# Performance work log

Hardware: AMD Instinct MI355X
Metric: run time of the kernel (lower is better)

The kernel has to match this reference:

```python
import jax, jax.numpy as jnp
import numpy as np

D = 4
P_PIX = 13   # 2*R+1, R=6
R_PIX = 6
P_REG = 7    # R+1
DIRATE = 2   # min(4, (20-0)//15 + 1) for ref_index=[0,18], current_ind=20, dil_int=15


def correlate(t, r, P, d):
    """SpatialCorrelationSampler(kernel_size=1, patch_size=P, dilation_patch=d).
    t, r: [b,c,h,w] -> [b,P*P,h,w] ; corr[n=(i*P+j)] uses r shifted by ((i-R)*d,(j-R)*d)."""
    b, c, h, w = t.shape
    Rr = (P - 1) // 2
    pad = Rr * d
    rp = jnp.pad(r, ((0, 0), (0, 0), (pad, pad), (pad, pad)))
    # [b,c,N,h,w] stack of shifted views (zero-padded borders)
    shifts = jnp.stack([rp[:, :, i * d:i * d + h, j * d:j * d + w]
                        for i in range(P) for j in range(P)], axis=2)
    return jnp.einsum('bcyx,bcnyx->bnyx', t, shifts)


def deform_im2col(r, offset, P):
    """Deformable im2col with one shared (x,y) offset per output pixel.
    r: [b,c,h,w], offset: [b,h,w,2] (x in [...,0], y in [...,1]) -> [b,c,P*P,h,w].
    Bilinear sampling with zero outside the image."""
    b, c, h, w = r.shape
    Rr = (P - 1) // 2
    N = P * P
    ky, kx = jnp.meshgrid(jnp.arange(-Rr, Rr + 1), jnp.arange(-Rr, Rr + 1), indexing='ij')
    ky = ky.reshape(-1).astype(r.dtype)
    kx = kx.reshape(-1).astype(r.dtype)
    ys = jnp.arange(h, dtype=r.dtype)
    xs = jnp.arange(w, dtype=r.dtype)
    sy = offset[..., 1][:, None] + ys[None, None, :, None] + ky[None, :, None, None]  # [b,N,h,w]
    sx = offset[..., 0][:, None] + xs[None, None, None, :] + kx[None, :, None, None]
    y0 = jnp.floor(sy)
    x0 = jnp.floor(sx)
    wy = sy - y0
    wx = sx - x0
    rf = r.reshape(b, c, h * w)

    def gather(yi, xi):
        valid = ((yi >= 0) & (yi < h) & (xi >= 0) & (xi < w)).astype(r.dtype)
        idx = (jnp.clip(yi, 0, h - 1).astype(jnp.int32) * w
               + jnp.clip(xi, 0, w - 1).astype(jnp.int32)).reshape(b, 1, -1)
        vals = jnp.take_along_axis(rf, jnp.broadcast_to(idx, (b, c, N * h * w)), axis=2)
        return vals.reshape(b, c, N, h, w), valid

    v00, m00 = gather(y0, x0)
    v01, m01 = gather(y0, x0 + 1)
    v10, m10 = gather(y0 + 1, x0)
    v11, m11 = gather(y0 + 1, x0 + 1)
    w00 = ((1 - wy) * (1 - wx) * m00)[:, None]
    w01 = ((1 - wy) * wx * m01)[:, None]
    w10 = (wy * (1 - wx) * m10)[:, None]
    w11 = (wy * wx * m11)[:, None]
    return v00 * w00 + v01 * w01 + v10 * w10 + v11 * w11


def unfold(x, P):
    """F.unfold(x, kernel_size=P, padding=(P-1)//2) -> [b,c,P*P,h,w]."""
    b, c, h, w = x.shape
    Rr = (P - 1) // 2
    xp = jnp.pad(x, ((0, 0), (0, 0), (Rr, Rr), (Rr, Rr)))
    return jnp.stack([xp[:, :, i:i + h, j:j + w]
                      for i in range(P) for j in range(P)], axis=2)


def setup_inputs() -> dict:
    key = jax.random.key(0)
    ks = jax.random.split(key, 8)
    inp = {
        'feats_r0': jax.random.normal(ks[0], (2, 128, 32, 32), jnp.float32),
        'feats_r1': jax.random.normal(ks[1], (2, 128, 32, 32), jnp.float32),
        'feats_t': jax.random.normal(ks[2], (2, 128, 32, 32), jnp.float32),
        'quantized_r0': jax.random.uniform(ks[3], (2, 3, 128, 128), jnp.float32),
        'quantized_r1': jax.random.uniform(ks[4], (2, 3, 128, 128), jnp.float32),
        'feats_r_semantic0': jax.random.normal(ks[5], (2, 512, 16, 16), jnp.float32),
        'feats_r_semantic1': jax.random.normal(ks[6], (2, 512, 16, 16), jnp.float32),
        'feats_t_semantic': jax.random.normal(ks[7], (2, 512, 16, 16), jnp.float32),
        'current_ind': 20,
    }
    return inp


def reference(feats_r0, feats_r1, feats_t, quantized_r0, quantized_r1,
              feats_r_semantic0, feats_r_semantic1, feats_t_semantic, current_ind):
    b, c, h, w = feats_t.shape
    b_, c_, h_, w_ = feats_t_semantic.shape
    P, Rr, N = P_PIX, R_PIX, P_PIX * P_PIX

    # --- searching ref 0 (far in time): dilated coarse correlation -> soft offset ---
    coarse = correlate(feats_t, feats_r0, P, DIRATE)                     # [b,N,h,w]
    cs = jax.nn.softmax(coarse.reshape(b, N, h * w), axis=1).reshape(b, P, P, h, w)
    gv = jnp.arange(-Rr, Rr + 1, dtype=feats_t.dtype)
    off_x = jnp.einsum('bijyx,j->byx', cs, gv) * DIRATE
    off_y = jnp.einsum('bijyx,i->byx', cs, gv) * DIRATE
    offset = jnp.stack([off_x, off_y], axis=-1)                          # [b,h,w,2]

    col0 = deform_im2col(feats_r0, offset, P)                            # [b,c,N,h,w]
    corr0 = jnp.einsum('bcyx,bcnyx->bnyx', feats_t, col0).reshape(b, N, h * w)

    # --- recent ref 1: plain pixel + region correlation ---
    corr1 = correlate(feats_t, feats_r1, P, 1).reshape(b, N, h * w)
    region = correlate(feats_t_semantic, feats_r_semantic1, P_REG, 1).reshape(b_, P_REG * P_REG, h_ * w_)
    corr = jax.nn.softmax(region, axis=1)[:, None]                       # [b,1,49,h_*w_]

    corr_pixel = jax.nn.softmax(jnp.concatenate([corr0, corr1], axis=1), axis=1)[:, None]  # [b,1,2N,hw]

    # --- propagate colors ---
    qr0 = quantized_r0[:, :, ::D, ::D]
    qr1 = quantized_r1[:, :, ::D, ::D]
    uf0 = deform_im2col(qr0, offset, P).reshape(b, 3, N, h * w)
    uf1 = unfold(qr1, P).reshape(b, 3, N, h * w)
    image_uf = jnp.concatenate([uf0, uf1], axis=2)                       # [b,3,2N,hw]
    out = (corr_pixel * image_uf).sum(2).reshape(b, 3, h, w)
    return (out, corr)
```

## Files before the change

kernel.cpp:

```cpp
#include <hip/hip_runtime.h>
#include <math.h>

#define HH 32
#define WW 32
#define CC 128
#define PPIX 13
#define RPIX 6
#define NPIX 169
#define G14 14
#define NG 196
#define NTOT 338
#define DIRATE_ 2
#define HS 16
#define WSz 16
#define CS 512
#define PREG 7
#define RREG 3
#define NREG 49
#define QH 128
#define MAIN_BLOCKS 2048
#define REG_BLOCKS 512

__device__ __forceinline__ float wave_sum(float v) {
    #pragma unroll
    for (int s = 1; s < 64; s <<= 1) v += __shfl_xor(v, s, 64);
    return v;
}
__device__ __forceinline__ float wave_max(float v) {
    #pragma unroll
    for (int s = 1; s < 64; s <<= 1) v = fmaxf(v, __shfl_xor(v, s, 64));
    return v;
}

__global__ __launch_bounds__(256) void prep(
    const float* __restrict__ fr0, const float* __restrict__ fr1,
    const float* __restrict__ ft,  const float* __restrict__ qr0,
    const float* __restrict__ qr1, const float* __restrict__ rs1,
    const float* __restrict__ ts,
    float* __restrict__ Tr0, float* __restrict__ Tr1, float* __restrict__ Tt,
    float* __restrict__ Trs1, float* __restrict__ Tts,
    float* __restrict__ qs0, float* __restrict__ qs1)
{
    __shared__ float tile[32][33];
    const int tid = threadIdx.x;
    const int tx = tid & 31, ty = tid >> 5;
    int bid = blockIdx.x;
    if (bid < 768) {
        const int t = bid >> 8, rem = bid & 255;
        const int p0 = (rem & 31) * 32;
        const int c0 = ((rem >> 5) & 3) * 32;
        const int b  = rem >> 7;
        const float* s = (t==0 ? fr0 : t==1 ? fr1 : ft) + (size_t)b*CC*1024;
        float* d       = (t==0 ? Tr0 : t==1 ? Tr1 : Tt) + (size_t)b*CC*1024;
        #pragma unroll
        for (int i = ty; i < 32; i += 8) tile[i][tx] = s[(size_t)(c0+i)*1024 + p0+tx];
        __syncthreads();
        #pragma unroll
        for (int i = ty; i < 32; i += 8) d[(size_t)(p0+i)*CC + c0+tx] = tile[tx][i];
    } else if (bid < 1280) {
        bid -= 768;
        const int t = bid >> 8, rem = bid & 255;
        const int p0 = (rem & 7) * 32;
        const int c0 = ((rem >> 3) & 15) * 32;
        const int b  = rem >> 7;
        const float* s = (t==0 ? rs1 : ts) + (size_t)b*CS*256;
        float* d       = (t==0 ? Trs1 : Tts) + (size_t)b*CS*256;
        #pragma unroll
        for (int i = ty; i < 32; i += 8) tile[i][tx] = s[(size_t)(c0+i)*256 + p0+tx];
        __syncthreads();
        #pragma unroll
        for (int i = ty; i < 32; i += 8) d[(size_t)(p0+i)*CS + c0+tx] = tile[tx][i];
    } else {
        const int base = (bid - 1280) * 256 + tid;
        for (int e = base; e < 2*6144; e += 2048) {
            const int t = e / 6144, r2 = e % 6144;
            const int bc = r2 >> 10, yx = r2 & 1023;
            const int yy = yx >> 5, xx = yx & 31;
            const float v = (t==0 ? qr0 : qr1)[((size_t)bc*QH + yy*4)*QH + xx*4];
            (t==0 ? qs0 : qs1)[r2] = v;
        }
    }
}

__global__ __launch_bounds__(512) void colorizer_fused(
    const float* __restrict__ Tr0,
    const float* __restrict__ Tr1,
    const float* __restrict__ Tt,
    const float* __restrict__ qs0,
    const float* __restrict__ qs1,
    const float* __restrict__ Trs1,
    const float* __restrict__ Tts,
    float* __restrict__ out,
    float* __restrict__ corr_out)
{
    __shared__ __align__(16) float tvec[CS];
    __shared__ float rbuf[72];
    __shared__ float smC0[NPIX];
    __shared__ float smG[NG];
    __shared__ float smC1[NPIX];
    __shared__ float smV[NTOT];
    __shared__ float smQ0[3*NG];
    __shared__ float smQ1[3*NPIX];

    const int tid  = threadIdx.x;
    const int lane = tid & 63;
    const int wid  = tid >> 6;

    if (blockIdx.x >= REG_BLOCKS) {
        const int orig = blockIdx.x - REG_BLOCKS;
        const int bid = (orig & 7) * (MAIN_BLOCKS/8) + (orig >> 3);
        const int b   = bid >> 10;
        const int pix = bid & 1023;
        const int y = pix >> 5, x = pix & 31;

        if (tid < 32)
            ((float4*)tvec)[tid] = ((const float4*)Tt)[(size_t)b*32768 + pix*32 + tid];
        __syncthreads();

        const float4* tp  = (const float4*)tvec;
        const float4* Tr0q = (const float4*)Tr0 + (size_t)b*32768;
        const float4* Tr1q = (const float4*)Tr1 + (size_t)b*32768;
        const int q4 = lane & 3, g4 = lane >> 2;

        float4 tf[8];
        #pragma unroll
        for (int r = 0; r < 8; ++r) tf[r] = tp[q4 + r*4];

        #pragma unroll 1
        for (int set = 0; set < 2; ++set) {
            const int di = set*128 + wid*16 + g4;
            int inb = 0, yx = 0;
            if (di < NPIX) {
                const int ys = y + (di/PPIX - RPIX)*DIRATE_;
                const int xs = x + (di%PPIX - RPIX)*DIRATE_;
                inb = (ys>=0 && ys<HH && xs>=0 && xs<WW);
                yx = inb ? ys*WW+xs : 0;
            }
            const float4* rp = Tr0q + yx*32 + q4;
            float4 a; a.x=a.y=a.z=a.w=0.f;
            #pragma unroll
            for (int r = 0; r < 8; ++r) {
                const float4 rv = rp[r*4];
                a.x = fmaf(rv.x,tf[r].x,a.x); a.y = fmaf(rv.y,tf[r].y,a.y);
                a.z = fmaf(rv.z,tf[r].z,a.z); a.w = fmaf(rv.w,tf[r].w,a.w);
            }
            float s = (a.x+a.y)+(a.z+a.w);
            s += __shfl_xor(s, 1, 64); s += __shfl_xor(s, 2, 64);
            if (q4 == 0 && di < NPIX) smC0[di] = inb ? s : 0.f;
        }
        __syncthreads();

        const float dv = (tid < NPIX) ? smC0[tid] : 0.f;
        {
            float wm = wave_max(tid < NPIX ? dv : -INFINITY);
            if (lane == 0) rbuf[wid] = wm;
        }
        __syncthreads();
        float M1 = rbuf[0];
        #pragma unroll
        for (int i = 1; i < 8; ++i) M1 = fmaxf(M1, rbuf[i]);
        {
            const float e   = (tid < NPIX) ? __expf(dv - M1) : 0.f;
            const float gvj = (tid < NPIX) ? (float)(tid % PPIX - RPIX) : 0.f;
            const float gvi = (tid < NPIX) ? (float)(tid / PPIX - RPIX) : 0.f;
            float s0 = wave_sum(e), s1 = wave_sum(e*gvj), s2 = wave_sum(e*gvi);
            if (lane == 0) { rbuf[8+wid] = s0; rbuf[16+wid] = s1; rbuf[24+wid] = s2; }
        }
        __syncthreads();
        float ssum = 0.f, sx = 0.f, sy = 0.f;
        #pragma unroll
        for (int i = 0; i < 8; ++i) { ssum += rbuf[8+i]; sx += rbuf[16+i]; sy += rbuf[24+i]; }
        const float off_x = sx / ssum * (float)DIRATE_;
        const float off_y = sy / ssum * (float)DIRATE_;

        const float fy = (float)y + off_y, fx = (float)x + off_x;
        const float fly = floorf(fy), flx = floorf(fx);
        const int yb = (int)fly - RPIX, xb = (int)flx - RPIX;
        const float wy = fy - fly, wx = fx - flx;
        const float w00 = (1.f-wy)*(1.f-wx), w01 = (1.f-wy)*wx;
        const float w10 = wy*(1.f-wx),       w11 = wy*wx;

        #pragma unroll 1
        for (int set = 0; set < 3; ++set) {
            const int di = set*128 + wid*16 + g4;
            const float4* basep = Tr0q;
            int inb = 0, yx = 0;
            if (di < NG) {
                const int ys = yb + di/G14, xs = xb + di%G14;
                inb = (ys>=0 && ys<HH && xs>=0 && xs<WW);
                yx = inb ? ys*WW+xs : 0;
            } else if (di < NG+NPIX) {
                const int k = di - NG;
                const int ys = y + k/PPIX - RPIX, xs = x + k%PPIX - RPIX;
                inb = (ys>=0 && ys<HH && xs>=0 && xs<WW);
                yx = inb ? ys*WW+xs : 0;
                basep = Tr1q;
            }
            const float4* rp = basep + yx*32 + q4;
            float4 a; a.x=a.y=a.z=a.w=0.f;
            #pragma unroll
            for (int r = 0; r < 8; ++r) {
                const float4 rv = rp[r*4];
                a.x = fmaf(rv.x,tf[r].x,a.x); a.y = fmaf(rv.y,tf[r].y,a.y);
                a.z = fmaf(rv.z,tf[r].z,a.z); a.w = fmaf(rv.w,tf[r].w,a.w);
            }
            float s = (a.x+a.y)+(a.z+a.w);
            s += __shfl_xor(s, 1, 64); s += __shfl_xor(s, 2, 64);
            if (q4 == 0 && di < NG+NPIX) {
                if (di < NG) smG[di] = inb ? s : 0.f;
                else         smC1[di-NG] = inb ? s : 0.f;
            }
        }
        for (int idx = tid; idx < 3*NG; idx += 512) {
            const int ch = idx / NG, a2 = idx % NG;
            const int ys = yb + a2 / G14, xs = xb + a2 % G14;
            smQ0[idx] = (ys>=0 && ys<HH && xs>=0 && xs<WW)
                        ? qs0[(b*3+ch)*1024 + ys*WW + xs] : 0.f;
        }
        for (int idx = tid; idx < 3*NPIX; idx += 512) {
            const int ch = idx / NPIX, a2 = idx % NPIX;
            const int ys = y + a2 / PPIX - RPIX, xs = x + a2 % PPIX - RPIX;
            smQ1[idx] = (ys>=0 && ys<HH && xs>=0 && xs<WW)
                        ? qs1[(b*3+ch)*1024 + ys*WW + xs] : 0.f;
        }
        __syncthreads();

        if (tid < NTOT) {
            float v;
            if (tid < NPIX) {
                const int i = tid / PPIX, j = tid % PPIX;
                const int g = i*G14 + j;
                v = w00*smG[g] + w01*smG[g+1] + w10*smG[g+G14] + w11*smG[g+G14+1];
            } else {
                v = smC1[tid - NPIX];
            }
            smV[tid] = v;
        }
        __syncthreads();

        const float ml = (tid < NTOT) ? smV[tid] : -INFINITY;
        {
            float wm = wave_max(ml);
            if (lane == 0) rbuf[32+wid] = wm;
        }
        __syncthreads();
        float M2 = rbuf[32];
        #pragma unroll
        for (int i = 1; i < 8; ++i) M2 = fmaxf(M2, rbuf[32+i]);

        float dpart = 0.f, o0 = 0.f, o1 = 0.f, o2 = 0.f;
        if (tid < NTOT) {
            const float ee = __expf(ml - M2);
            dpart = ee;
            if (tid < NPIX) {
                const int i = tid / PPIX, j = tid % PPIX;
                const int g = i*G14 + j;
                o0 = ee * (w00*smQ0[g]          + w01*smQ0[g+1]
                         + w10*smQ0[g+G14]      + w11*smQ0[g+G14+1]);
                o1 = ee * (w00*smQ0[NG+g]       + w01*smQ0[NG+g+1]
                         + w10*smQ0[NG+g+G14]   + w11*smQ0[NG+g+G14+1]);
                o2 = ee * (w00*smQ0[2*NG+g]     + w01*smQ0[2*NG+g+1]
                         + w10*smQ0[2*NG+g+G14] + w11*smQ0[2*NG+g+G14+1]);
            } else {
                const int k = tid - NPIX;
                o0 = ee * smQ1[k];
                o1 = ee * smQ1[NPIX + k];
                o2 = ee * smQ1[2*NPIX + k];
            }
        }
        {
            float s0 = wave_sum(dpart), s1 = wave_sum(o0), s2 = wave_sum(o1), s3 = wave_sum(o2);
            if (lane == 0) { rbuf[40+wid]=s0; rbuf[48+wid]=s1; rbuf[56+wid]=s2; rbuf[64+wid]=s3; }
        }
        __syncthreads();
        if (tid == 0) {
            float denom=0.f, r0s=0.f, r1s=0.f, r2s=0.f;
            #pragma unroll
            for (int i = 0; i < 8; ++i) {
                denom += rbuf[40+i]; r0s += rbuf[48+i]; r1s += rbuf[56+i]; r2s += rbuf[64+i];
            }
            const float inv = 1.f / denom;
            out[((b*3+0)*HH + y)*WW + x] = r0s * inv;
            out[((b*3+1)*HH + y)*WW + x] = r1s * inv;
            out[((b*3+2)*HH + y)*WW + x] = r2s * inv;
        }
    } else {
        const int rb0 = blockIdx.x;
        const int rb  = (rb0 & 7) * (REG_BLOCKS/8) + (rb0 >> 3);
        const int b   = rb >> 8;
        const int pix = rb & 255;
        const int y = pix >> 4, x = pix & 15;

        if (tid < 128)
            ((float4*)tvec)[tid] = ((const float4*)Tts)[(size_t)b*32768 + pix*128 + tid];
        __syncthreads();

        const float4* tp  = (const float4*)tvec;
        const float4* Tsq = (const float4*)Trs1 + (size_t)b*32768;
        const int q8 = lane & 7, g8 = lane >> 3;

        const int di = wid*8 + g8;
        int inb = 0, yx = 0;
        if (di < NREG) {
            const int ys = y + di/PREG - RREG, xs = x + di%PREG - RREG;
            inb = (ys>=0 && ys<HS && xs>=0 && xs<WSz);
            yx = inb ? ys*WSz+xs : 0;
        }
        const float4* rp = Tsq + yx*128 + q8;
        float4 a; a.x=a.y=a.z=a.w=0.f;
        #pragma unroll 8
        for (int r = 0; r < 16; ++r) {
            const float4 rv = rp[r*8];
            const float4 tv = tp[q8 + r*8];
            a.x = fmaf(rv.x,tv.x,a.x); a.y = fmaf(rv.y,tv.y,a.y);
            a.z = fmaf(rv.z,tv.z,a.z); a.w = fmaf(rv.w,tv.w,a.w);
        }
        float s = (a.x+a.y)+(a.z+a.w);
        s += __shfl_xor(s, 1, 64); s += __shfl_xor(s, 2, 64); s += __shfl_xor(s, 4, 64);
        if (q8 == 0 && di < NREG) smG[di] = inb ? s : 0.f;
        __syncthreads();

        if (wid == 0) {
            const bool act = lane < NREG;
            const float val = act ? smG[lane] : -INFINITY;
            const float M = wave_max(val);
            const float e = act ? __expf(val - M) : 0.f;
            const float ssum = wave_sum(e);
            if (act) corr_out[b*NREG*(HS*WSz) + lane*(HS*WSz) + pix] = e / ssum;
        }
    }
}

extern "C" void kernel_launch(void* const* d_in, const int* in_sizes, int n_in,
                              void* d_out, int out_size, void* d_ws, size_t ws_size,
                              hipStream_t stream) {
    const float* feats_r0 = (const float*)d_in[0];
    const float* feats_r1 = (const float*)d_in[1];
    const float* feats_t  = (const float*)d_in[2];
    const float* q_r0     = (const float*)d_in[3];
    const float* q_r1     = (const float*)d_in[4];
    const float* rs1      = (const float*)d_in[6];
    const float* ts       = (const float*)d_in[7];

    float* ws = (float*)d_ws;
    float* Tr0  = ws;
    float* Tr1  = Tr0  + 262144;
    float* Tt   = Tr1  + 262144;
    float* Trs1 = Tt   + 262144;
    float* Tts  = Trs1 + 262144;
    float* qs0  = Tts  + 262144;
    float* qs1  = qs0  + 6144;

    prep<<<1288, 256, 0, stream>>>(feats_r0, feats_r1, feats_t, q_r0, q_r1,
                                   rs1, ts, Tr0, Tr1, Tt, Trs1, Tts, qs0, qs1);

    float* out  = (float*)d_out;
    float* corr = out + 2*3*HH*WW;

    colorizer_fused<<<MAIN_BLOCKS + REG_BLOCKS, 512, 0, stream>>>(
        Tr0, Tr1, Tt, qs0, qs1, Trs1, Tts, out, corr);
}
```

Baseline: 112.6 us.

## Move corr1 and quantized ref1 loads before offset softmax; use per-wave reductions

The corr1 dot products and the smQ1 color gather now run in the same first pass as corr0, before the offset softmax, so the dependent deformable pass only computes the 196 grid entries and needs two sets instead of three. Each wave now reduces the offset softmax (169 values) and the final max over 338 logits redundantly on its own, which removes several block-wide barriers and rbuf round-trips. The final sum loop reads only 6 waves, since threads 384+ contribute nothing. This trades some redundant per-wave LDS reads and exp work for fewer __syncthreads and a shorter serial dependency chain.

```diff
diff --git a/kernel.cpp b/kernel.cpp
--- a/kernel.cpp
+++ b/kernel.cpp
@@ -94,7 +94,7 @@
     float* __restrict__ corr_out)
 {
     __shared__ __align__(16) float tvec[CS];
-    __shared__ float rbuf[72];
+    __shared__ float rbuf[32];
     __shared__ float smC0[NPIX];
     __shared__ float smG[NG];
     __shared__ float smC1[NPIX];
@@ -127,12 +127,75 @@
         for (int r = 0; r < 8; ++r) tf[r] = tp[q4 + r*4];
 
         #pragma unroll 1
-        for (int set = 0; set < 2; ++set) {
+        for (int set = 0; set < 3; ++set) {
             const int di = set*128 + wid*16 + g4;
+            const float4* basep = Tr0q;
             int inb = 0, yx = 0;
             if (di < NPIX) {
                 const int ys = y + (di/PPIX - RPIX)*DIRATE_;
                 const int xs = x + (di%PPIX - RPIX)*DIRATE_;
+                inb = (ys>=0 && ys<HH && xs>=0 && xs<WW);
+                yx = inb ? ys*WW+xs : 0;
+            } else if (di < NTOT) {
+                const int k = di - NPIX;
+                const int ys = y + k/PPIX - RPIX, xs = x + k%PPIX - RPIX;
+                inb = (ys>=0 && ys<HH && xs>=0 && xs<WW);
+                yx = inb ? ys*WW+xs : 0;
+                basep = Tr1q;
+            }
+            const float4* rp = basep + yx*32 + q4;
+            float4 a; a.x=a.y=a.z=a.w=0.f;
+            #pragma unroll
+            for (int r = 0; r < 8; ++r) {
+                const float4 rv = rp[r*4];
+                a.x = fmaf(rv.x,tf[r].x,a.x); a.y = fmaf(rv.y,tf[r].y,a.y);
+                a.z = fmaf(rv.z,tf[r].z,a.z); a.w = fmaf(rv.w,tf[r].w,a.w);
+            }
+            float s = (a.x+a.y)+(a.z+a.w);
+            s += __shfl_xor(s, 1, 64); s += __shfl_xor(s, 2, 64);
+            if (q4 == 0 && di < NTOT) {
+                if (di < NPIX) smC0[di] = inb ? s : 0.f;
+                else           smC1[di-NPIX] = inb ? s : 0.f;
+            }
+        }
+        if (tid < 3*NPIX) {
+            const int ch = tid / NPIX, a2 = tid % NPIX;
+            const int ys = y + a2 / PPIX - RPIX, xs = x + a2 % PPIX - RPIX;
+            smQ1[tid] = (ys>=0 && ys<HH && xs>=0 && xs<WW)
+                        ? qs1[(b*3+ch)*1024 + ys*WW + xs] : 0.f;
+        }
+        __syncthreads();
+
+        const int l1 = lane + 64, l2 = lane + 128;
+        const float v0 = smC0[lane];
+        const float v1 = (l1 < NPIX) ? smC0[l1] : -INFINITY;
+        const float v2 = (l2 < NPIX) ? smC0[l2] : -INFINITY;
+        const float M1 = wave_max(fmaxf(v0, fmaxf(v1, v2)));
+        const float e0 = __expf(v0 - M1);
+        const float e1 = (l1 < NPIX) ? __expf(v1 - M1) : 0.f;
+        const float e2 = (l2 < NPIX) ? __expf(v2 - M1) : 0.f;
+        const float gj0 = (float)(lane % PPIX - RPIX), gi0 = (float)(lane / PPIX - RPIX);
+        const float gj1 = (float)(l1 % PPIX - RPIX),   gi1 = (float)(l1 / PPIX - RPIX);
+        const float gj2 = (float)(l2 % PPIX - RPIX),   gi2 = (float)(l2 / PPIX - RPIX);
+        const float ssum = wave_sum(e0 + e1 + e2);
+        const float sx   = wave_sum(e0*gj0 + e1*gj1 + e2*gj2);
+        const float sy   = wave_sum(e0*gi0 + e1*gi1 + e2*gi2);
+        const float off_x = sx / ssum * (float)DIRATE_;
+        const float off_y = sy / ssum * (float)DIRATE_;
+
+        const float fy = (float)y + off_y, fx = (float)x + off_x;
+        const float fly = floorf(fy), flx = floorf(fx);
+        const int yb = (int)fly - RPIX, xb = (int)flx - RPIX;
+        const float wy = fy - fly, wx = fx - flx;
+        const float w00 = (1.f-wy)*(1.f-wx), w01 = (1.f-wy)*wx;
+        const float w10 = wy*(1.f-wx),       w11 = wy*wx;
+
+        #pragma unroll 1
+        for (int set = 0; set < 2; ++set) {
+            const int di = set*128 + wid*16 + g4;
+            int inb = 0, yx = 0;
+            if (di < NG) {
+                const int ys = yb + di/G14, xs = xb + di%G14;
                 inb = (ys>=0 && ys<HH && xs>=0 && xs<WW);
                 yx = inb ? ys*WW+xs : 0;
             }
@@ -146,82 +209,13 @@
             }
             float s = (a.x+a.y)+(a.z+a.w);
             s += __shfl_xor(s, 1, 64); s += __shfl_xor(s, 2, 64);
-            if (q4 == 0 && di < NPIX) smC0[di] = inb ? s : 0.f;
-        }
-        __syncthreads();
-
-        const float dv = (tid < NPIX) ? smC0[tid] : 0.f;
-        {
-            float wm = wave_max(tid < NPIX ? dv : -INFINITY);
-            if (lane == 0) rbuf[wid] = wm;
-        }
-        __syncthreads();
-        float M1 = rbuf[0];
-        #pragma unroll
-        for (int i = 1; i < 8; ++i) M1 = fmaxf(M1, rbuf[i]);
-        {
-            const float e   = (tid < NPIX) ? __expf(dv - M1) : 0.f;
-            const float gvj = (tid < NPIX) ? (float)(tid % PPIX - RPIX) : 0.f;
-            const float gvi = (tid < NPIX) ? (float)(tid / PPIX - RPIX) : 0.f;
-            float s0 = wave_sum(e), s1 = wave_sum(e*gvj), s2 = wave_sum(e*gvi);
-            if (lane == 0) { rbuf[8+wid] = s0; rbuf[16+wid] = s1; rbuf[24+wid] = s2; }
-        }
-        __syncthreads();
-        float ssum = 0.f, sx = 0.f, sy = 0.f;
-        #pragma unroll
-        for (int i = 0; i < 8; ++i) { ssum += rbuf[8+i]; sx += rbuf[16+i]; sy += rbuf[24+i]; }
-        const float off_x = sx / ssum * (float)DIRATE_;
-        const float off_y = sy / ssum * (float)DIRATE_;
-
-        const float fy = (float)y + off_y, fx = (float)x + off_x;
-        const float fly = floorf(fy), flx = floorf(fx);
-        const int yb = (int)fly - RPIX, xb = (int)flx - RPIX;
-        const float wy = fy - fly, wx = fx - flx;
-        const float w00 = (1.f-wy)*(1.f-wx), w01 = (1.f-wy)*wx;
-        const float w10 = wy*(1.f-wx),       w11 = wy*wx;
-
-        #pragma unroll 1
-        for (int set = 0; set < 3; ++set) {
-            const int di = set*128 + wid*16 + g4;
-            const float4* basep = Tr0q;
-            int inb = 0, yx = 0;
-            if (di < NG) {
-                const int ys = yb + di/G14, xs = xb + di%G14;
-                inb = (ys>=0 && ys<HH && xs>=0 && xs<WW);
-                yx = inb ? ys*WW+xs : 0;
-            } else if (di < NG+NPIX) {
-                const int k = di - NG;
-                const int ys = y + k/PPIX - RPIX, xs = x + k%PPIX - RPIX;
-                inb = (ys>=0 && ys<HH && xs>=0 && xs<WW);
-                yx = inb ? ys*WW+xs : 0;
-                basep = Tr1q;
-            }
-            const float4* rp = basep + yx*32 + q4;
-            float4 a; a.x=a.y=a.z=a.w=0.f;
-            #pragma unroll
-            for (int r = 0; r < 8; ++r) {
-                const float4 rv = rp[r*4];
-                a.x = fmaf(rv.x,tf[r].x,a.x); a.y = fmaf(rv.y,tf[r].y,a.y);
-                a.z = fmaf(rv.z,tf[r].z,a.z); a.w = fmaf(rv.w,tf[r].w,a.w);
-            }
-            float s = (a.x+a.y)+(a.z+a.w);
-            s += __shfl_xor(s, 1, 64); s += __shfl_xor(s, 2, 64);
-            if (q4 == 0 && di < NG+NPIX) {
-                if (di < NG) smG[di] = inb ? s : 0.f;
-                else         smC1[di-NG] = inb ? s : 0.f;
-            }
+            if (q4 == 0 && di < NG) smG[di] = inb ? s : 0.f;
         }
         for (int idx = tid; idx < 3*NG; idx += 512) {
             const int ch = idx / NG, a2 = idx % NG;
             const int ys = yb + a2 / G14, xs = xb + a2 % G14;
             smQ0[idx] = (ys>=0 && ys<HH && xs>=0 && xs<WW)
                         ? qs0[(b*3+ch)*1024 + ys*WW + xs] : 0.f;
-        }
-        for (int idx = tid; idx < 3*NPIX; idx += 512) {
-            const int ch = idx / NPIX, a2 = idx % NPIX;
-            const int ys = y + a2 / PPIX - RPIX, xs = x + a2 % PPIX - RPIX;
-            smQ1[idx] = (ys>=0 && ys<HH && xs>=0 && xs<WW)
-                        ? qs1[(b*3+ch)*1024 + ys*WW + xs] : 0.f;
         }
         __syncthreads();
 
@@ -238,19 +232,14 @@
         }
         __syncthreads();
 
-        const float ml = (tid < NTOT) ? smV[tid] : -INFINITY;
-        {
-            float wm = wave_max(ml);
-            if (lane == 0) rbuf[32+wid] = wm;
-        }
-        __syncthreads();
-        float M2 = rbuf[32];
-        #pragma unroll
-        for (int i = 1; i < 8; ++i) M2 = fmaxf(M2, rbuf[32+i]);
+        float ml = smV[lane];
+        #pragma unroll
+        for (int k = lane + 64; k < NTOT; k += 64) ml = fmaxf(ml, smV[k]);
+        const float M2 = wave_max(ml);
 
         float dpart = 0.f, o0 = 0.f, o1 = 0.f, o2 = 0.f;
         if (tid < NTOT) {
-            const float ee = __expf(ml - M2);
+            const float ee = __expf(smV[tid] - M2);
             dpart = ee;
             if (tid < NPIX) {
                 const int i = tid / PPIX, j = tid % PPIX;
@@ -270,14 +259,14 @@
         }
         {
             float s0 = wave_sum(dpart), s1 = wave_sum(o0), s2 = wave_sum(o1), s3 = wave_sum(o2);
-            if (lane == 0) { rbuf[40+wid]=s0; rbuf[48+wid]=s1; rbuf[56+wid]=s2; rbuf[64+wid]=s3; }
+            if (lane == 0) { rbuf[wid]=s0; rbuf[8+wid]=s1; rbuf[16+wid]=s2; rbuf[24+wid]=s3; }
         }
         __syncthreads();
         if (tid == 0) {
             float denom=0.f, r0s=0.f, r1s=0.f, r2s=0.f;
             #pragma unroll
-            for (int i = 0; i < 8; ++i) {
-                denom += rbuf[40+i]; r0s += rbuf[48+i]; r1s += rbuf[56+i]; r2s += rbuf[64+i];
+            for (int i = 0; i < 6; ++i) {
+                denom += rbuf[i]; r0s += rbuf[8+i]; r1s += rbuf[16+i]; r2s += rbuf[24+i];
             }
             const float inv = 1.f / denom;
             out[((b*3+0)*HH + y)*WW + x] = r0s * inv;
```

Result: faster. 110.3 us (-2.0%).
